# Kernel tuning notes

Hardware: AMD Instinct MI355X
Metric: run time of the kernel (lower is better)

Reference implementation:

```python
import jax, jax.numpy as jnp
import numpy as np

B, NM, D, H = 16384, 5, 256, 8
LN_EPS = 1e-5


def _ln(x, g, b):
    m = jnp.mean(x, axis=-1, keepdims=True)
    v = jnp.var(x, axis=-1, keepdims=True)
    return (x - m) / jnp.sqrt(v + LN_EPS) * g + b


def _mha(q_in, kv_in, Wi, bi, Wo, bo):
    # q_in: [B,1,D], kv_in: [B,1,D]; Wi: [3D,D] packed q/k/v like nn.MultiheadAttention
    Bq, Lq, Dm = q_in.shape
    Lk = kv_in.shape[1]
    dh = Dm // H
    q = (q_in @ Wi[:Dm].T + bi[:Dm]).reshape(Bq, Lq, H, dh).transpose(0, 2, 1, 3)
    k = (kv_in @ Wi[Dm:2 * Dm].T + bi[Dm:2 * Dm]).reshape(Bq, Lk, H, dh).transpose(0, 2, 1, 3)
    v = (kv_in @ Wi[2 * Dm:].T + bi[2 * Dm:]).reshape(Bq, Lk, H, dh).transpose(0, 2, 1, 3)
    scores = jnp.einsum('bhqd,bhkd->bhqk', q, k) * (1.0 / np.sqrt(dh))
    attn = jax.nn.softmax(scores, axis=-1)  # trivially 1.0 for Lk=1, kept for fidelity
    out = jnp.einsum('bhqk,bhkd->bhqd', attn, v).transpose(0, 2, 1, 3).reshape(Bq, Lq, Dm)
    return out @ Wo.T + bo


def setup_inputs() -> dict:
    key = jax.random.key(0)
    ks = jax.random.split(key, 8)
    s = 0.02
    return {
        'x': jax.random.normal(ks[0], (B, NM, D), jnp.float32),
        'self_Wi': jax.random.normal(ks[1], (3 * D, D), jnp.float32) * s,
        'self_bi': jnp.zeros((3 * D,), jnp.float32),
        'self_Wo': jax.random.normal(ks[2], (D, D), jnp.float32) * s,
        'self_bo': jnp.zeros((D,), jnp.float32),
        'cross_Wi': jax.random.normal(ks[3], (4, 3 * D, D), jnp.float32) * s,
        'cross_bi': jnp.zeros((4, 3 * D), jnp.float32),
        'cross_Wo': jax.random.normal(ks[4], (4, D, D), jnp.float32) * s,
        'cross_bo': jnp.zeros((4, D), jnp.float32),
        'cross_ln_g': jnp.ones((4, D), jnp.float32),
        'cross_ln_b': jnp.zeros((4, D), jnp.float32),
        'gate_ln_g': jnp.ones((D,), jnp.float32),
        'gate_ln_b': jnp.zeros((D,), jnp.float32),
        'gate_W': jax.random.normal(ks[5], (NM, D), jnp.float32) * s,
        'gate_b': jnp.zeros((NM,), jnp.float32),
        'final_ln_g': jnp.ones((D,), jnp.float32),
        'final_ln_b': jnp.zeros((D,), jnp.float32),
        'modal_idx': 2,
    }


def reference(x, self_Wi, self_bi, self_Wo, self_bo,
              cross_Wi, cross_bi, cross_Wo, cross_bo, cross_ln_g, cross_ln_b,
              gate_ln_g, gate_ln_b, gate_W, gate_b, final_ln_g, final_ln_b,
              modal_idx):
    query = x[:, modal_idx:modal_idx + 1, :]  # [B,1,D]
    self_out = _mha(query, query, self_Wi, self_bi, self_Wo, self_bo)

    other_idx = [i for i in range(NM) if i != modal_idx]
    kv = jnp.swapaxes(x[:, other_idx, :], 0, 1)[:, :, None, :]  # [4,B,1,D]

    def branch(Wi, bi, Wo, bo, g, b, kv_i):
        a = _mha(query, kv_i, Wi, bi, Wo, bo)
        return _ln(query + a, g, b)  # dropout is identity in eval

    cross_outs = jax.vmap(branch)(cross_Wi, cross_bi, cross_Wo, cross_bo,
                                  cross_ln_g, cross_ln_b, kv)  # [4,B,1,D]

    gates = jax.nn.softmax(_ln(query, gate_ln_g, gate_ln_b) @ gate_W.T + gate_b, axis=-1)  # [B,1,5]
    combined = gates[..., 0:1] * self_out + jnp.einsum('nbld,bln->bld', cross_outs, gates[..., 1:])
    return _ln(query + combined, final_ln_g, final_ln_b)
```

## Files before the change

kernel.cpp:

```cpp
#include <hip/hip_runtime.h>


typedef __attribute__((ext_vector_type(8))) short short8;
typedef __attribute__((ext_vector_type(4))) float floatx4;

__device__ __forceinline__ float b2f(unsigned short h) {
    union { unsigned int u; float f; } v; v.u = ((unsigned int)h) << 16; return v.f;
}
__device__ __forceinline__ unsigned short f2b(float f) {
    union { unsigned int u; float f; } v; v.f = f;
    unsigned int u = v.u;
    return (unsigned short)((u + 0x7FFFu + ((u >> 16) & 1u)) >> 16);
}

__global__ __launch_bounds__(256) void k_fuse(
    const float* __restrict__ sWi, const float* __restrict__ sbi,
    const float* __restrict__ sWo, const float* __restrict__ sbo,
    const float* __restrict__ cWi, const float* __restrict__ cbi,
    const float* __restrict__ cWo, const float* __restrict__ cbo,
    unsigned short* __restrict__ WF, float* __restrict__ BF)
{
    int s = blockIdx.y;
    int i0 = blockIdx.x * 4;
    int tid = threadIdx.x;
    const float *Wo, *Wv, *bv, *bo;
    if (s == 0) { Wo = sWo; Wv = sWi + 512 * 256; bv = sbi + 512; bo = sbo; }
    else {
        int n = s - 1;
        Wo = cWo + n * 65536;
        Wv = cWi + n * 768 * 256 + 512 * 256;
        bv = cbi + n * 768 + 512;
        bo = cbo + n * 256;
    }
    __shared__ float wo[4 * 256];
    #pragma unroll
    for (int it = 0; it < 4; ++it) {
        int idx = tid + it * 256;
        wo[idx] = Wo[i0 * 256 + idx];
    }
    __syncthreads();
    float a0 = 0.f, a1 = 0.f, a2 = 0.f, a3 = 0.f;
    for (int k = 0; k < 256; ++k) {
        float wv = Wv[k * 256 + tid];
        a0 += wo[k] * wv;
        a1 += wo[256 + k] * wv;
        a2 += wo[512 + k] * wv;
        a3 += wo[768 + k] * wv;
    }
    unsigned short* dst = WF + ((size_t)s * 256 + i0) * 256 + tid;
    dst[0] = f2b(a0); dst[256] = f2b(a1); dst[512] = f2b(a2); dst[768] = f2b(a3);
    if (tid < 4) {
        int i = i0 + tid;
        float bacc = 0.f;
        for (int k = 0; k < 256; ++k) bacc += Wo[i * 256 + k] * bv[k];
        BF[s * 256 + i] = bacc + bo[i];
    }
}

__device__ __forceinline__ float wred(float v) {
    #pragma unroll
    for (int o = 32; o > 0; o >>= 1) v += __shfl_xor(v, o, 64);
    return v;
}

__global__ __launch_bounds__(256) void k_main(
    const float* __restrict__ x, const unsigned short* __restrict__ WF,
    const float* __restrict__ BF,
    const float* __restrict__ cln_g, const float* __restrict__ cln_b,
    const float* __restrict__ gln_g, const float* __restrict__ gln_b,
    const float* __restrict__ gW, const float* __restrict__ gb,
    const float* __restrict__ fln_g, const float* __restrict__ fln_b,
    const int* __restrict__ midx, float* __restrict__ out)
{
    __shared__ __align__(16) unsigned short A[32 * 264];
    __shared__ __align__(16) unsigned short Yb[32 * 264];
    __shared__ float gWs[5 * 256];
    __shared__ float gLDS[32 * 8];

    int m = midx[0];
    int b0 = blockIdx.x * 32;
    int tid = threadIdx.x;
    int wave = tid >> 6, lane = tid & 63;
    int l16 = lane & 15, q4 = lane >> 4;
    int j = lane * 4;

    #pragma unroll
    for (int i = 0; i < 5; ++i) gWs[tid + i * 256] = gW[tid + i * 256];

    float qv[8][4];
    #pragma unroll
    for (int rr = 0; rr < 8; ++rr) {
        int r = wave * 8 + rr;
        float4 u = *(const float4*)(x + ((size_t)(b0 + r) * 5 + m) * 256 + j);
        qv[rr][0] = u.x; qv[rr][1] = u.y; qv[rr][2] = u.z; qv[rr][3] = u.w;
    }
    float4 glg = *(const float4*)(gln_g + j);
    float4 glb = *(const float4*)(gln_b + j);
    float gbv[5];
    #pragma unroll
    for (int n = 0; n < 5; ++n) gbv[n] = gb[n];

    __syncthreads();

    #pragma unroll
    for (int rr = 0; rr < 8; ++rr) {
        int r = wave * 8 + rr;
        float s1 = wred(qv[rr][0] + qv[rr][1] + qv[rr][2] + qv[rr][3]);
        float s2 = wred(qv[rr][0]*qv[rr][0] + qv[rr][1]*qv[rr][1] +
                        qv[rr][2]*qv[rr][2] + qv[rr][3]*qv[rr][3]);
        float mn = s1 * (1.f / 256.f);
        float vr = s2 * (1.f / 256.f) - mn * mn;
        float rs = rsqrtf(vr + 1e-5f);
        float qln[4];
        qln[0] = (qv[rr][0] - mn) * rs * glg.x + glb.x;
        qln[1] = (qv[rr][1] - mn) * rs * glg.y + glb.y;
        qln[2] = (qv[rr][2] - mn) * rs * glg.z + glb.z;
        qln[3] = (qv[rr][3] - mn) * rs * glg.w + glb.w;
        float g[5];
        #pragma unroll
        for (int n = 0; n < 5; ++n) {
            float p = qln[0] * gWs[n * 256 + j] + qln[1] * gWs[n * 256 + j + 1]
                    + qln[2] * gWs[n * 256 + j + 2] + qln[3] * gWs[n * 256 + j + 3];
            g[n] = wred(p) + gbv[n];
        }
        float mx = g[0];
        #pragma unroll
        for (int n = 1; n < 5; ++n) mx = fmaxf(mx, g[n]);
        float es = 0.f;
        #pragma unroll
        for (int n = 0; n < 5; ++n) { g[n] = __expf(g[n] - mx); es += g[n]; }
        float inv = 1.f / es;
        if (lane == 0) {
            #pragma unroll
            for (int n = 0; n < 5; ++n) gLDS[r * 8 + n] = g[n] * inv;
        }
    }

    float comb[8][4];
    #pragma unroll
    for (int rr = 0; rr < 8; ++rr)
        #pragma unroll
        for (int i = 0; i < 4; ++i) comb[rr][i] = 0.f;

    for (int s = 0; s < 5; ++s) {
        int mod = (s == 0) ? m : ((s - 1 < m) ? s - 1 : s);
        #pragma unroll
        for (int it = 0; it < 8; ++it) {
            int c = tid + it * 256;
            int row = c >> 6;
            int c4 = (c & 63) << 2;
            float4 v = *(const float4*)(x + ((size_t)(b0 + row) * 5 + mod) * 256 + c4);
            uint2 p;
            p.x = (unsigned int)f2b(v.x) | ((unsigned int)f2b(v.y) << 16);
            p.y = (unsigned int)f2b(v.z) | ((unsigned int)f2b(v.w) << 16);
            *(uint2*)(&A[row * 264 + c4]) = p;
        }
        __syncthreads();

        floatx4 acc[2][4];
        #pragma unroll
        for (int rt = 0; rt < 2; ++rt)
            #pragma unroll
            for (int ct = 0; ct < 4; ++ct) acc[rt][ct] = (floatx4){0.f, 0.f, 0.f, 0.f};
        const unsigned short* wB = WF + (size_t)s * 65536;
        #pragma unroll
        for (int kk = 0; kk < 8; ++kk) {
            int k = kk * 32 + q4 * 8;
            short8 a0 = *(const short8*)(&A[l16 * 264 + k]);
            short8 a1 = *(const short8*)(&A[(16 + l16) * 264 + k]);
            short8 bb[4];
            #pragma unroll
            for (int ct = 0; ct < 4; ++ct)
                bb[ct] = *(const short8*)(wB + (size_t)(wave * 64 + ct * 16 + l16) * 256 + k);
            #pragma unroll
            for (int ct = 0; ct < 4; ++ct) {
                acc[0][ct] = __builtin_amdgcn_mfma_f32_16x16x32_bf16(a0, bb[ct], acc[0][ct], 0, 0, 0);
                acc[1][ct] = __builtin_amdgcn_mfma_f32_16x16x32_bf16(a1, bb[ct], acc[1][ct], 0, 0, 0);
            }
        }
        #pragma unroll
        for (int rt = 0; rt < 2; ++rt)
            #pragma unroll
            for (int i = 0; i < 4; ++i) {
                int r = rt * 16 + q4 * 4 + i;
                #pragma unroll
                for (int ct = 0; ct < 4; ++ct)
                    Yb[r * 264 + wave * 64 + ct * 16 + l16] = f2b(acc[rt][ct][i]);
            }
        __syncthreads();

        float4 bfv = *(const float4*)(BF + s * 256 + j);
        if (s == 0) {
            #pragma unroll
            for (int rr = 0; rr < 8; ++rr) {
                int r = wave * 8 + rr;
                uint2 u = *(const uint2*)(&Yb[r * 264 + j]);
                float y0 = b2f(u.x & 0xffff) + bfv.x, y1 = b2f(u.x >> 16) + bfv.y;
                float y2 = b2f(u.y & 0xffff) + bfv.z, y3 = b2f(u.y >> 16) + bfv.w;
                float g0 = gLDS[r * 8 + 0];
                comb[rr][0] += g0 * y0; comb[rr][1] += g0 * y1;
                comb[rr][2] += g0 * y2; comb[rr][3] += g0 * y3;
            }
        } else {
            float4 cg = *(const float4*)(cln_g + (s - 1) * 256 + j);
            float4 cb = *(const float4*)(cln_b + (s - 1) * 256 + j);
            #pragma unroll
            for (int rr = 0; rr < 8; ++rr) {
                int r = wave * 8 + rr;
                uint2 u = *(const uint2*)(&Yb[r * 264 + j]);
                float t0 = qv[rr][0] + b2f(u.x & 0xffff) + bfv.x;
                float t1 = qv[rr][1] + b2f(u.x >> 16)    + bfv.y;
                float t2 = qv[rr][2] + b2f(u.y & 0xffff) + bfv.z;
                float t3 = qv[rr][3] + b2f(u.y >> 16)    + bfv.w;
                float s1 = wred(t0 + t1 + t2 + t3);
                float s2 = wred(t0*t0 + t1*t1 + t2*t2 + t3*t3);
                float mn = s1 * (1.f / 256.f);
                float vr = s2 * (1.f / 256.f) - mn * mn;
                float rs = rsqrtf(vr + 1e-5f);
                float gs = gLDS[r * 8 + s];
                comb[rr][0] += gs * ((t0 - mn) * rs * cg.x + cb.x);
                comb[rr][1] += gs * ((t1 - mn) * rs * cg.y + cb.y);
                comb[rr][2] += gs * ((t2 - mn) * rs * cg.z + cb.z);
                comb[rr][3] += gs * ((t3 - mn) * rs * cg.w + cb.w);
            }
        }
    }

    float4 fg = *(const float4*)(fln_g + j);
    float4 fb = *(const float4*)(fln_b + j);
    #pragma unroll
    for (int rr = 0; rr < 8; ++rr) {
        int r = wave * 8 + rr;
        float t0 = qv[rr][0] + comb[rr][0], t1 = qv[rr][1] + comb[rr][1];
        float t2 = qv[rr][2] + comb[rr][2], t3 = qv[rr][3] + comb[rr][3];
        float s1 = wred(t0 + t1 + t2 + t3);
        float s2 = wred(t0*t0 + t1*t1 + t2*t2 + t3*t3);
        float mn = s1 * (1.f / 256.f);
        float vr = s2 * (1.f / 256.f) - mn * mn;
        float rs = rsqrtf(vr + 1e-5f);
        float4 ov;
        ov.x = (t0 - mn) * rs * fg.x + fb.x;
        ov.y = (t1 - mn) * rs * fg.y + fb.y;
        ov.z = (t2 - mn) * rs * fg.z + fb.z;
        ov.w = (t3 - mn) * rs * fg.w + fb.w;
        *(float4*)(out + (size_t)(b0 + r) * 256 + j) = ov;
    }
}

extern "C" void kernel_launch(void* const* d_in, const int* in_sizes, int n_in,
                              void* d_out, int out_size, void* d_ws, size_t ws_size,
                              hipStream_t stream) {
    const float* x    = (const float*)d_in[0];
    const float* sWi  = (const float*)d_in[1];
    const float* sbi  = (const float*)d_in[2];
    const float* sWo  = (const float*)d_in[3];
    const float* sbo  = (const float*)d_in[4];
    const float* cWi  = (const float*)d_in[5];
    const float* cbi  = (const float*)d_in[6];
    const float* cWo  = (const float*)d_in[7];
    const float* cbo  = (const float*)d_in[8];
    const float* clng = (const float*)d_in[9];
    const float* clnb = (const float*)d_in[10];
    const float* glng = (const float*)d_in[11];
    const float* glnb = (const float*)d_in[12];
    const float* gW   = (const float*)d_in[13];
    const float* gb   = (const float*)d_in[14];
    const float* flng = (const float*)d_in[15];
    const float* flnb = (const float*)d_in[16];
    const int* midx   = (const int*)d_in[17];
    float* out        = (float*)d_out;

    char* ws = (char*)d_ws;
    unsigned short* WF = (unsigned short*)ws;
    float* BF          = (float*)(ws + 655360);

    k_fuse<<<dim3(64, 5), 256, 0, stream>>>(sWi, sbi, sWo, sbo, cWi, cbi, cWo, cbo, WF, BF);
    k_main<<<512, 256, 0, stream>>>(x, WF, BF, clng, clnb, glng, glnb, gW, gb, flng, flnb, midx, out);
}
```

Measured before the change: 225.2 us.

## Keep MFMA outputs in registers, double-buffer activation tiles, halve rows per block

The main kernel now processes 16 rows per block over 1024 blocks instead of 32 rows over 512. LayerNorm and gating are computed directly on the MFMA accumulator layout, with cross-wave partial sums exchanged through small LDS arrays, so the bf16 Y staging buffer and its round trip are removed. The next modality's x tile is prefetched into registers and written to a second LDS buffer while the current GEMM runs, and launch bounds request 4 blocks per CU. In k_fuse, the bias fold is spread over a whole wave with a shuffle reduction rather than 4 serial threads, and the inner loop is unrolled. The trade-off is more cross-wave synchronisation and each block reloading the full weight matrix for only 16 rows.

```diff
diff --git a/kernel.cpp b/kernel.cpp
--- a/kernel.cpp
+++ b/kernel.cpp
@@ -40,6 +40,7 @@
     }
     __syncthreads();
     float a0 = 0.f, a1 = 0.f, a2 = 0.f, a3 = 0.f;
+    #pragma unroll 8
     for (int k = 0; k < 256; ++k) {
         float wv = Wv[k * 256 + tid];
         a0 += wo[k] * wv;
@@ -49,21 +50,21 @@
     }
     unsigned short* dst = WF + ((size_t)s * 256 + i0) * 256 + tid;
     dst[0] = f2b(a0); dst[256] = f2b(a1); dst[512] = f2b(a2); dst[768] = f2b(a3);
-    if (tid < 4) {
-        int i = i0 + tid;
-        float bacc = 0.f;
-        for (int k = 0; k < 256; ++k) bacc += Wo[i * 256 + k] * bv[k];
-        BF[s * 256 + i] = bacc + bo[i];
-    }
-}
-
-__device__ __forceinline__ float wred(float v) {
-    #pragma unroll
-    for (int o = 32; o > 0; o >>= 1) v += __shfl_xor(v, o, 64);
-    return v;
-}
-
-__global__ __launch_bounds__(256) void k_main(
+    int wv_ = tid >> 6, ln = tid & 63;
+    float p = 0.f;
+    #pragma unroll
+    for (int u = 0; u < 4; ++u) {
+        int k = ln * 4 + u;
+        p += wo[wv_ * 256 + k] * bv[k];
+    }
+    #pragma unroll
+    for (int o = 32; o > 0; o >>= 1) p += __shfl_xor(p, o, 64);
+    if (ln == 0) BF[s * 256 + i0 + wv_] = p + bo[i0 + wv_];
+}
+
+#define ASTR 280
+
+__global__ __launch_bounds__(256, 4) void k_main(
     const float* __restrict__ x, const unsigned short* __restrict__ WF,
     const float* __restrict__ BF,
     const float* __restrict__ cln_g, const float* __restrict__ cln_b,
@@ -72,56 +73,97 @@
     const float* __restrict__ fln_g, const float* __restrict__ fln_b,
     const int* __restrict__ midx, float* __restrict__ out)
 {
-    __shared__ __align__(16) unsigned short A[32 * 264];
-    __shared__ __align__(16) unsigned short Yb[32 * 264];
-    __shared__ float gWs[5 * 256];
-    __shared__ float gLDS[32 * 8];
-
-    int m = midx[0];
-    int b0 = blockIdx.x * 32;
-    int tid = threadIdx.x;
-    int wave = tid >> 6, lane = tid & 63;
-    int l16 = lane & 15, q4 = lane >> 4;
-    int j = lane * 4;
-
-    #pragma unroll
-    for (int i = 0; i < 5; ++i) gWs[tid + i * 256] = gW[tid + i * 256];
-
-    float qv[8][4];
-    #pragma unroll
-    for (int rr = 0; rr < 8; ++rr) {
-        int r = wave * 8 + rr;
-        float4 u = *(const float4*)(x + ((size_t)(b0 + r) * 5 + m) * 256 + j);
-        qv[rr][0] = u.x; qv[rr][1] = u.y; qv[rr][2] = u.z; qv[rr][3] = u.w;
-    }
-    float4 glg = *(const float4*)(gln_g + j);
-    float4 glb = *(const float4*)(gln_b + j);
-    float gbv[5];
-    #pragma unroll
-    for (int n = 0; n < 5; ++n) gbv[n] = gb[n];
-
-    __syncthreads();
-
-    #pragma unroll
-    for (int rr = 0; rr < 8; ++rr) {
-        int r = wave * 8 + rr;
-        float s1 = wred(qv[rr][0] + qv[rr][1] + qv[rr][2] + qv[rr][3]);
-        float s2 = wred(qv[rr][0]*qv[rr][0] + qv[rr][1]*qv[rr][1] +
-                        qv[rr][2]*qv[rr][2] + qv[rr][3]*qv[rr][3]);
+    __shared__ __align__(16) unsigned short Ab[2][16 * ASTR];
+    __shared__ float2 st2[16 * 4];
+    __shared__ float stN[5][16 * 4];
+    __shared__ float gLDS[16 * 8];
+
+    const int m = midx[0];
+    const int b0 = blockIdx.x * 16;
+    const int tid = threadIdx.x;
+    const int wave = tid >> 6, lane = tid & 63;
+    const int l16 = lane & 15, q4 = lane >> 4;
+    const int colb = wave * 64;
+
+    float4 sreg[4];
+    #pragma unroll
+    for (int it = 0; it < 4; ++it) {
+        int c = tid + it * 256;
+        sreg[it] = *(const float4*)(x + ((size_t)(b0 + (c >> 6)) * 5 + m) * 256 + ((c & 63) << 2));
+    }
+
+    float qv[4][4];
+    #pragma unroll
+    for (int i = 0; i < 4; ++i)
+        #pragma unroll
+        for (int ct = 0; ct < 4; ++ct)
+            qv[i][ct] = x[((size_t)(b0 + q4 * 4 + i) * 5 + m) * 256 + colb + ct * 16 + l16];
+    float glgv[4], glbv[4];
+    #pragma unroll
+    for (int ct = 0; ct < 4; ++ct) {
+        glgv[ct] = gln_g[colb + ct * 16 + l16];
+        glbv[ct] = gln_b[colb + ct * 16 + l16];
+    }
+
+    #pragma unroll
+    for (int it = 0; it < 4; ++it) {
+        int c = tid + it * 256;
+        float4 v = sreg[it];
+        uint2 p;
+        p.x = (unsigned int)f2b(v.x) | ((unsigned int)f2b(v.y) << 16);
+        p.y = (unsigned int)f2b(v.z) | ((unsigned int)f2b(v.w) << 16);
+        *(uint2*)(&Ab[0][(c >> 6) * ASTR + ((c & 63) << 2)]) = p;
+    }
+    __syncthreads();
+
+    #pragma unroll
+    for (int i = 0; i < 4; ++i) {
+        float p1 = qv[i][0] + qv[i][1] + qv[i][2] + qv[i][3];
+        float p2 = qv[i][0]*qv[i][0] + qv[i][1]*qv[i][1] + qv[i][2]*qv[i][2] + qv[i][3]*qv[i][3];
+        #pragma unroll
+        for (int o = 1; o < 16; o <<= 1) { p1 += __shfl_xor(p1, o, 64); p2 += __shfl_xor(p2, o, 64); }
+        if (l16 == 0) st2[(q4 * 4 + i) * 4 + wave] = make_float2(p1, p2);
+    }
+    __syncthreads();
+    float qln[4][4];
+    #pragma unroll
+    for (int i = 0; i < 4; ++i) {
+        float s1 = 0.f, s2 = 0.f;
+        #pragma unroll
+        for (int w2 = 0; w2 < 4; ++w2) { float2 v = st2[(q4 * 4 + i) * 4 + w2]; s1 += v.x; s2 += v.y; }
         float mn = s1 * (1.f / 256.f);
         float vr = s2 * (1.f / 256.f) - mn * mn;
         float rs = rsqrtf(vr + 1e-5f);
-        float qln[4];
-        qln[0] = (qv[rr][0] - mn) * rs * glg.x + glb.x;
-        qln[1] = (qv[rr][1] - mn) * rs * glg.y + glb.y;
-        qln[2] = (qv[rr][2] - mn) * rs * glg.z + glb.z;
-        qln[3] = (qv[rr][3] - mn) * rs * glg.w + glb.w;
+        #pragma unroll
+        for (int ct = 0; ct < 4; ++ct) qln[i][ct] = (qv[i][ct] - mn) * rs * glgv[ct] + glbv[ct];
+    }
+    #pragma unroll
+    for (int n = 0; n < 5; ++n) {
+        float pg[4];
+        #pragma unroll
+        for (int i = 0; i < 4; ++i) {
+            float acc = 0.f;
+            #pragma unroll
+            for (int ct = 0; ct < 4; ++ct) acc += qln[i][ct] * gW[n * 256 + colb + ct * 16 + l16];
+            #pragma unroll
+            for (int o = 1; o < 16; o <<= 1) acc += __shfl_xor(acc, o, 64);
+            pg[i] = acc;
+        }
+        if (l16 == 0) {
+            #pragma unroll
+            for (int i = 0; i < 4; ++i) stN[n][(q4 * 4 + i) * 4 + wave] = pg[i];
+        }
+    }
+    __syncthreads();
+    if (wave == 0 && lane < 16) {
+        int r = lane;
         float g[5];
         #pragma unroll
         for (int n = 0; n < 5; ++n) {
-            float p = qln[0] * gWs[n * 256 + j] + qln[1] * gWs[n * 256 + j + 1]
-                    + qln[2] * gWs[n * 256 + j + 2] + qln[3] * gWs[n * 256 + j + 3];
-            g[n] = wred(p) + gbv[n];
+            float sum = gb[n];
+            #pragma unroll
+            for (int w2 = 0; w2 < 4; ++w2) sum += stN[n][r * 4 + w2];
+            g[n] = sum;
         }
         float mx = g[0];
         #pragma unroll
@@ -130,120 +172,142 @@
         #pragma unroll
         for (int n = 0; n < 5; ++n) { g[n] = __expf(g[n] - mx); es += g[n]; }
         float inv = 1.f / es;
-        if (lane == 0) {
-            #pragma unroll
-            for (int n = 0; n < 5; ++n) gLDS[r * 8 + n] = g[n] * inv;
-        }
-    }
-
-    float comb[8][4];
-    #pragma unroll
-    for (int rr = 0; rr < 8; ++rr)
-        #pragma unroll
-        for (int i = 0; i < 4; ++i) comb[rr][i] = 0.f;
-
+        #pragma unroll
+        for (int n = 0; n < 5; ++n) gLDS[r * 8 + n] = g[n] * inv;
+    }
+    __syncthreads();
+
+    float comb[4][4];
+    #pragma unroll
+    for (int i = 0; i < 4; ++i)
+        #pragma unroll
+        for (int ct = 0; ct < 4; ++ct) comb[i][ct] = 0.f;
+
+    int cur = 0;
     for (int s = 0; s < 5; ++s) {
-        int mod = (s == 0) ? m : ((s - 1 < m) ? s - 1 : s);
-        #pragma unroll
-        for (int it = 0; it < 8; ++it) {
-            int c = tid + it * 256;
-            int row = c >> 6;
-            int c4 = (c & 63) << 2;
-            float4 v = *(const float4*)(x + ((size_t)(b0 + row) * 5 + mod) * 256 + c4);
-            uint2 p;
-            p.x = (unsigned int)f2b(v.x) | ((unsigned int)f2b(v.y) << 16);
-            p.y = (unsigned int)f2b(v.z) | ((unsigned int)f2b(v.w) << 16);
-            *(uint2*)(&A[row * 264 + c4]) = p;
-        }
-        __syncthreads();
-
-        floatx4 acc[2][4];
-        #pragma unroll
-        for (int rt = 0; rt < 2; ++rt)
-            #pragma unroll
-            for (int ct = 0; ct < 4; ++ct) acc[rt][ct] = (floatx4){0.f, 0.f, 0.f, 0.f};
+        float bfv[4], cgv[4], cbv[4], gsv[4];
+        #pragma unroll
+        for (int ct = 0; ct < 4; ++ct) {
+            int col = colb + ct * 16 + l16;
+            bfv[ct] = BF[s * 256 + col];
+            if (s > 0) {
+                cgv[ct] = cln_g[(s - 1) * 256 + col];
+                cbv[ct] = cln_b[(s - 1) * 256 + col];
+            } else { cgv[ct] = 0.f; cbv[ct] = 0.f; }
+        }
+        #pragma unroll
+        for (int i = 0; i < 4; ++i) gsv[i] = gLDS[(q4 * 4 + i) * 8 + s];
+
+        float4 nreg[4];
+        if (s < 4) {
+            int nmod = (s < m) ? s : s + 1;
+            #pragma unroll
+            for (int it = 0; it < 4; ++it) {
+                int c = tid + it * 256;
+                nreg[it] = *(const float4*)(x + ((size_t)(b0 + (c >> 6)) * 5 + nmod) * 256 + ((c & 63) << 2));
+            }
+        }
+
+        floatx4 acc[4];
+        #pragma unroll
+        for (int ct = 0; ct < 4; ++ct) acc[ct] = (floatx4){0.f, 0.f, 0.f, 0.f};
         const unsigned short* wB = WF + (size_t)s * 65536;
         #pragma unroll
         for (int kk = 0; kk < 8; ++kk) {
             int k = kk * 32 + q4 * 8;
-            short8 a0 = *(const short8*)(&A[l16 * 264 + k]);
-            short8 a1 = *(const short8*)(&A[(16 + l16) * 264 + k]);
-            short8 bb[4];
-            #pragma unroll
-            for (int ct = 0; ct < 4; ++ct)
-                bb[ct] = *(const short8*)(wB + (size_t)(wave * 64 + ct * 16 + l16) * 256 + k);
+            short8 a = *(const short8*)(&Ab[cur][l16 * ASTR + k]);
             #pragma unroll
             for (int ct = 0; ct < 4; ++ct) {
-                acc[0][ct] = __builtin_amdgcn_mfma_f32_16x16x32_bf16(a0, bb[ct], acc[0][ct], 0, 0, 0);
-                acc[1][ct] = __builtin_amdgcn_mfma_f32_16x16x32_bf16(a1, bb[ct], acc[1][ct], 0, 0, 0);
-            }
-        }
-        #pragma unroll
-        for (int rt = 0; rt < 2; ++rt)
+                short8 bb = *(const short8*)(wB + (size_t)(colb + ct * 16 + l16) * 256 + k);
+                acc[ct] = __builtin_amdgcn_mfma_f32_16x16x32_bf16(a, bb, acc[ct], 0, 0, 0);
+            }
+        }
+
+        float tv[4][4];
+        if (s == 0) {
+            #pragma unroll
+            for (int i = 0; i < 4; ++i)
+                #pragma unroll
+                for (int ct = 0; ct < 4; ++ct) tv[i][ct] = acc[ct][i] + bfv[ct];
+        } else {
             #pragma unroll
             for (int i = 0; i < 4; ++i) {
-                int r = rt * 16 + q4 * 4 + i;
-                #pragma unroll
-                for (int ct = 0; ct < 4; ++ct)
-                    Yb[r * 264 + wave * 64 + ct * 16 + l16] = f2b(acc[rt][ct][i]);
-            }
+                #pragma unroll
+                for (int ct = 0; ct < 4; ++ct) tv[i][ct] = qv[i][ct] + acc[ct][i] + bfv[ct];
+                float p1 = tv[i][0] + tv[i][1] + tv[i][2] + tv[i][3];
+                float p2 = tv[i][0]*tv[i][0] + tv[i][1]*tv[i][1] + tv[i][2]*tv[i][2] + tv[i][3]*tv[i][3];
+                #pragma unroll
+                for (int o = 1; o < 16; o <<= 1) { p1 += __shfl_xor(p1, o, 64); p2 += __shfl_xor(p2, o, 64); }
+                if (l16 == 0) st2[(q4 * 4 + i) * 4 + wave] = make_float2(p1, p2);
+            }
+        }
+
+        if (s < 4) {
+            #pragma unroll
+            for (int it = 0; it < 4; ++it) {
+                int c = tid + it * 256;
+                float4 v = nreg[it];
+                uint2 p;
+                p.x = (unsigned int)f2b(v.x) | ((unsigned int)f2b(v.y) << 16);
+                p.y = (unsigned int)f2b(v.z) | ((unsigned int)f2b(v.w) << 16);
+                *(uint2*)(&Ab[cur ^ 1][(c >> 6) * ASTR + ((c & 63) << 2)]) = p;
+            }
+        }
         __syncthreads();
 
-        float4 bfv = *(const float4*)(BF + s * 256 + j);
         if (s == 0) {
             #pragma unroll
-            for (int rr = 0; rr < 8; ++rr) {
-                int r = wave * 8 + rr;
-                uint2 u = *(const uint2*)(&Yb[r * 264 + j]);
-                float y0 = b2f(u.x & 0xffff) + bfv.x, y1 = b2f(u.x >> 16) + bfv.y;
-                float y2 = b2f(u.y & 0xffff) + bfv.z, y3 = b2f(u.y >> 16) + bfv.w;
-                float g0 = gLDS[r * 8 + 0];
-                comb[rr][0] += g0 * y0; comb[rr][1] += g0 * y1;
-                comb[rr][2] += g0 * y2; comb[rr][3] += g0 * y3;
-            }
+            for (int i = 0; i < 4; ++i)
+                #pragma unroll
+                for (int ct = 0; ct < 4; ++ct) comb[i][ct] += gsv[i] * tv[i][ct];
         } else {
-            float4 cg = *(const float4*)(cln_g + (s - 1) * 256 + j);
-            float4 cb = *(const float4*)(cln_b + (s - 1) * 256 + j);
-            #pragma unroll
-            for (int rr = 0; rr < 8; ++rr) {
-                int r = wave * 8 + rr;
-                uint2 u = *(const uint2*)(&Yb[r * 264 + j]);
-                float t0 = qv[rr][0] + b2f(u.x & 0xffff) + bfv.x;
-                float t1 = qv[rr][1] + b2f(u.x >> 16)    + bfv.y;
-                float t2 = qv[rr][2] + b2f(u.y & 0xffff) + bfv.z;
-                float t3 = qv[rr][3] + b2f(u.y >> 16)    + bfv.w;
-                float s1 = wred(t0 + t1 + t2 + t3);
-                float s2 = wred(t0*t0 + t1*t1 + t2*t2 + t3*t3);
+            #pragma unroll
+            for (int i = 0; i < 4; ++i) {
+                float s1 = 0.f, s2 = 0.f;
+                #pragma unroll
+                for (int w2 = 0; w2 < 4; ++w2) { float2 v = st2[(q4 * 4 + i) * 4 + w2]; s1 += v.x; s2 += v.y; }
                 float mn = s1 * (1.f / 256.f);
                 float vr = s2 * (1.f / 256.f) - mn * mn;
                 float rs = rsqrtf(vr + 1e-5f);
-                float gs = gLDS[r * 8 + s];
-                comb[rr][0] += gs * ((t0 - mn) * rs * cg.x + cb.x);
-                comb[rr][1] += gs * ((t1 - mn) * rs * cg.y + cb.y);
-                comb[rr][2] += gs * ((t2 - mn) * rs * cg.z + cb.z);
-                comb[rr][3] += gs * ((t3 - mn) * rs * cg.w + cb.w);
-            }
-        }
-    }
-
-    float4 fg = *(const float4*)(fln_g + j);
-    float4 fb = *(const float4*)(fln_b + j);
-    #pragma unroll
-    for (int rr = 0; rr < 8; ++rr) {
-        int r = wave * 8 + rr;
-        float t0 = qv[rr][0] + comb[rr][0], t1 = qv[rr][1] + comb[rr][1];
-        float t2 = qv[rr][2] + comb[rr][2], t3 = qv[rr][3] + comb[rr][3];
-        float s1 = wred(t0 + t1 + t2 + t3);
-        float s2 = wred(t0*t0 + t1*t1 + t2*t2 + t3*t3);
+                #pragma unroll
+                for (int ct = 0; ct < 4; ++ct)
+                    comb[i][ct] += gsv[i] * ((tv[i][ct] - mn) * rs * cgv[ct] + cbv[ct]);
+            }
+        }
+        __syncthreads();
+        cur ^= 1;
+    }
+
+    float fgv[4], fbv[4];
+    #pragma unroll
+    for (int ct = 0; ct < 4; ++ct) {
+        fgv[ct] = fln_g[colb + ct * 16 + l16];
+        fbv[ct] = fln_b[colb + ct * 16 + l16];
+    }
+    float tf[4][4];
+    #pragma unroll
+    for (int i = 0; i < 4; ++i) {
+        #pragma unroll
+        for (int ct = 0; ct < 4; ++ct) tf[i][ct] = qv[i][ct] + comb[i][ct];
+        float p1 = tf[i][0] + tf[i][1] + tf[i][2] + tf[i][3];
+        float p2 = tf[i][0]*tf[i][0] + tf[i][1]*tf[i][1] + tf[i][2]*tf[i][2] + tf[i][3]*tf[i][3];
+        #pragma unroll
+        for (int o = 1; o < 16; o <<= 1) { p1 += __shfl_xor(p1, o, 64); p2 += __shfl_xor(p2, o, 64); }
+        if (l16 == 0) st2[(q4 * 4 + i) * 4 + wave] = make_float2(p1, p2);
+    }
+    __syncthreads();
+    #pragma unroll
+    for (int i = 0; i < 4; ++i) {
+        float s1 = 0.f, s2 = 0.f;
+        #pragma unroll
+        for (int w2 = 0; w2 < 4; ++w2) { float2 v = st2[(q4 * 4 + i) * 4 + w2]; s1 += v.x; s2 += v.y; }
         float mn = s1 * (1.f / 256.f);
         float vr = s2 * (1.f / 256.f) - mn * mn;
         float rs = rsqrtf(vr + 1e-5f);
-        float4 ov;
-        ov.x = (t0 - mn) * rs * fg.x + fb.x;
-        ov.y = (t1 - mn) * rs * fg.y + fb.y;
-        ov.z = (t2 - mn) * rs * fg.z + fb.z;
-        ov.w = (t3 - mn) * rs * fg.w + fb.w;
-        *(float4*)(out + (size_t)(b0 + r) * 256 + j) = ov;
+        #pragma unroll
+        for (int ct = 0; ct < 4; ++ct)
+            out[(size_t)(b0 + q4 * 4 + i) * 256 + colb + ct * 16 + l16] =
+                (tf[i][ct] - mn) * rs * fgv[ct] + fbv[ct];
     }
 }
 
@@ -275,5 +339,5 @@
     float* BF          = (float*)(ws + 655360);
 
     k_fuse<<<dim3(64, 5), 256, 0, stream>>>(sWi, sbi, sWo, sbo, cWi, cbi, cWo, cbo, WF, BF);
-    k_main<<<512, 256, 0, stream>>>(x, WF, BF, clng, clnb, glng, glnb, gW, gb, flng, flnb, midx, out);
-}
+    k_main<<<1024, 256, 0, stream>>>(x, WF, BF, clng, clnb, glng, glnb, gW, gb, flng, flnb, midx, out);
+}
```

Result: slower. 293.6 us (+30.4%).
